# Optimization experiments

Hardware: AMD Instinct MI355X
Metric: run time of the kernel (lower is better)

Reference implementation:

```python
import jax, jax.numpy as jnp
import numpy as np

NUM_EXPERTS = 16
EFF_THRESHOLD = 0.1
SIM_THRESHOLD = 0.0
EPS = 1e-8


def setup_inputs() -> dict:
    key = jax.random.key(0)
    k1, k2 = jax.random.split(key)
    B, E, H = 4096, NUM_EXPERTS, 1024
    rp = jax.random.uniform(k1, (B, E), dtype=jnp.float32)
    rp = rp / rp.sum(axis=-1, keepdims=True)  # valid probabilities
    emb = jax.random.normal(k2, (B, H), dtype=jnp.float32)
    return {"routing_probs": rp, "input_embeddings": emb}


def _total_loss(routing_probs, input_embeddings):
    B, E = routing_probs.shape

    # --- LoadBalanceLoss: var(mean usage) / (1/E)^2, unbiased var (torch default)
    usage = routing_probs.mean(axis=0)                      # [E]
    var = jnp.sum((usage - usage.mean()) ** 2) / (E - 1)
    load_balance = var * (E ** 2)

    # --- EntropyRegularizationLoss (target None): -mean entropy
    entropy = -jnp.sum(routing_probs * jnp.log(routing_probs + EPS), axis=-1)
    entropy_loss = -entropy.mean()

    # --- EfficiencyLoss: sum of probs below threshold, averaged over batch
    small = jnp.where(routing_probs < EFF_THRESHOLD, routing_probs, 0.0)
    efficiency = small.sum(axis=-1).mean()

    # --- ConsistencyLoss: mean KL(softmax(p_j) || softmax(p_i)) over similar pairs
    logp = jax.nn.log_softmax(routing_probs, axis=-1)       # [B, E]
    q = jnp.exp(logp)                                       # [B, E]
    neg_ent_q = jnp.sum(q * logp, axis=-1)                  # [B], = sum q log q
    # KL[i, j] = sum_e q_j (log q_j - logp_i) = neg_ent_q[j] - logp_i . q_j
    kl = neg_ent_q[None, :] - jnp.einsum('ie,je->ij', logp, q)  # [B, B]

    nemb = input_embeddings / jnp.linalg.norm(input_embeddings, axis=-1, keepdims=True)
    sim = nemb @ nemb.T                                     # [B, B]
    mask = (sim > SIM_THRESHOLD) & (~jnp.eye(B, dtype=bool))
    num_pairs = mask.sum()
    cons_sum = jnp.sum(jnp.where(mask, kl, 0.0))
    consistency = jnp.where(num_pairs > 0,
                            cons_sum / jnp.maximum(num_pairs, 1).astype(kl.dtype),
                            0.0)

    return load_balance + entropy_loss + efficiency + consistency


def reference(routing_probs, input_embeddings):
    return _total_loss(routing_probs, input_embeddings)
```

## Files before the change

kernel.cpp:

```cpp
#include <hip/hip_runtime.h>
#include <hip/hip_bf16.h>

#define BROWS 4096
#define NE    16
#define HDIM  1024
#define ACC_F 128
#define NTILE 32
#define NBLK  (NTILE * (NTILE + 1) / 2)

typedef __attribute__((ext_vector_type(8))) short short8;
typedef __attribute__((ext_vector_type(4))) float float4v;

__device__ __forceinline__ unsigned bf16rne(float f) {
    const unsigned u = __float_as_uint(f);
    return (u + 0x7FFFu + ((u >> 16) & 1u)) >> 16;
}
__device__ __forceinline__ unsigned pk2(float lo, float hi) {
    return bf16rne(lo) | (bf16rne(hi) << 16);
}

__device__ __forceinline__ void row16f(const float* src, float* p) {
    const float4v* pv = (const float4v*)src;
    float4v a0 = pv[0], a1 = pv[1], a2 = pv[2], a3 = pv[3];
    p[0]=a0.x; p[1]=a0.y; p[2]=a0.z; p[3]=a0.w;
    p[4]=a1.x; p[5]=a1.y; p[6]=a1.z; p[7]=a1.w;
    p[8]=a2.x; p[9]=a2.y; p[10]=a2.z; p[11]=a2.w;
    p[12]=a3.x; p[13]=a3.y; p[14]=a3.z; p[15]=a3.w;
}

__device__ __forceinline__ void lsm16(const float* p, float* lp, float* q, float& ne) {
    float m = p[0];
#pragma unroll
    for (int e = 1; e < 16; e++) m = fmaxf(m, p[e]);
    float s = 0.f;
#pragma unroll
    for (int e = 0; e < 16; e++) s += expf(p[e] - m);
    const float ls = logf(s);
    ne = 0.f;
#pragma unroll
    for (int e = 0; e < 16; e++) {
        lp[e] = p[e] - m - ls;
        q[e]  = expf(lp[e]);
        ne   += q[e] * lp[e];
    }
}

__device__ __forceinline__ void ldsrow16(const float* base, float* r) {
    float4v a0 = *(const float4v*)(base);
    float4v a1 = *(const float4v*)(base + 4);
    float4v a2 = *(const float4v*)(base + 8);
    float4v a3 = *(const float4v*)(base + 12);
    r[0]=a0.x; r[1]=a0.y; r[2]=a0.z; r[3]=a0.w;
    r[4]=a1.x; r[5]=a1.y; r[6]=a1.z; r[7]=a1.w;
    r[8]=a2.x; r[9]=a2.y; r[10]=a2.z; r[11]=a2.w;
    r[12]=a3.x; r[13]=a3.y; r[14]=a3.z; r[15]=a3.w;
}

__global__ __launch_bounds__(256) void conv_init(
    const float* __restrict__ src, unsigned short* __restrict__ dst, float* __restrict__ acc)
{
    if (blockIdx.x == 0 && threadIdx.x < ACC_F) acc[threadIdx.x] = 0.f;
    const size_t i = ((size_t)blockIdx.x * 256 + threadIdx.x) * 8;
    float4v a = *(const float4v*)(src + i);
    float4v b = *(const float4v*)(src + i + 4);
    uint4 w = {pk2(a.x,a.y), pk2(a.z,a.w), pk2(b.x,b.y), pk2(b.z,b.w)};
    *(uint4*)(dst + i) = w;
}

__device__ __forceinline__ void decode_pair(int id, int& bi, int& bj) {
    int L = (id & 7) * 66 + (id >> 3);
    int gi = 0, gj = 0;
    for (;;) {
        const int cnt = (gi == gj) ? 10 : 16;
        if (L < cnt) break;
        L -= cnt;
        gj++; if (gj == 8) { gi++; gj = gi; }
    }
    if (gi == gj) {
        int u = 0, c = 4;
        while (L >= c) { L -= c; u++; c--; }
        bi = gi * 4 + u; bj = gj * 4 + u + L;
    } else {
        bi = gi * 4 + (L >> 2); bj = gj * 4 + (L & 3);
    }
}

template<bool PRE>
__global__ __launch_bounds__(512, 4) void gram_kl(
    const float* __restrict__ embf, const unsigned short* __restrict__ embb,
    const float* __restrict__ rp, float* __restrict__ acc,
    unsigned int* __restrict__ out)
{
    __shared__ char smem[40960];
    __shared__ float red[16];
    __shared__ int islast;
    __shared__ float fin[96];
    __hip_bfloat16* tA = (__hip_bfloat16*)smem;
    __hip_bfloat16* tB = (__hip_bfloat16*)(smem + 8192);
    float* lpI = (float*)smem;
    float* qI  = (float*)(smem + 10240);
    float* lpJ = (float*)(smem + 20480);
    float* qJ  = (float*)(smem + 30720);

    int bi, bj;
    decode_pair((int)blockIdx.x, bi, bj);

    const int t = threadIdx.x;
    const int lane = t & 63, wid = t >> 6;
    const int wi0 = (wid >> 1) * 32, wj0 = (wid & 1) * 64;
    const int lrow = lane & 15, quad = lane >> 4;

    const int row = t >> 2, cp = t & 3;
    const int sw  = cp ^ ((row >> 1) & 3);
    const int off = row * 32 + sw * 8;

    float4v accf[2][4];
#pragma unroll
    for (int a = 0; a < 2; a++)
#pragma unroll
        for (int b = 0; b < 4; b++) { accf[a][b].x=0.f; accf[a][b].y=0.f; accf[a][b].z=0.f; accf[a][b].w=0.f; }

    int roA[2], roB[4];
#pragma unroll
    for (int f = 0; f < 2; f++) {
        const int ra = wi0 + f * 16 + lrow;
        roA[f] = ra * 32 + (quad ^ ((ra >> 1) & 3)) * 8;
    }
#pragma unroll
    for (int f = 0; f < 4; f++) {
        const int rb = wj0 + f * 16 + lrow;
        roB[f] = rb * 32 + (quad ^ ((rb >> 1) & 3)) * 8;
    }

    if (PRE) {
        const unsigned short* gA = embb + (size_t)(bi * 128) * HDIM;
        const unsigned short* gB = embb + (size_t)(bj * 128) * HDIM;
        uint4 va = *(const uint4*)(gA + (size_t)row * HDIM + cp * 8);
        uint4 vb = *(const uint4*)(gB + (size_t)row * HDIM + cp * 8);
        for (int kt = 0; kt < HDIM; kt += 32) {
            __syncthreads();
            *(uint4*)(tA + off) = va;
            *(uint4*)(tB + off) = vb;
            __syncthreads();
            const int kn = (kt + 32 < HDIM) ? (kt + 32) : kt;
            va = *(const uint4*)(gA + (size_t)row * HDIM + kn + cp * 8);
            vb = *(const uint4*)(gB + (size_t)row * HDIM + kn + cp * 8);
            short8 a[2], b[4];
#pragma unroll
            for (int f = 0; f < 2; f++) a[f] = *(const short8*)(tA + roA[f]);
#pragma unroll
            for (int f = 0; f < 4; f++) b[f] = *(const short8*)(tB + roB[f]);
#pragma unroll
            for (int fi = 0; fi < 2; fi++)
#pragma unroll
                for (int fj = 0; fj < 4; fj++)
                    accf[fi][fj] = __builtin_amdgcn_mfma_f32_16x16x32_bf16(
                        a[fi], b[fj], accf[fi][fj], 0, 0, 0);
        }
    } else {
        const float* gA = embf + (size_t)(bi * 128) * HDIM;
        const float* gB = embf + (size_t)(bj * 128) * HDIM;
        float4v a0, a1, b0, b1;
        {
            const float* pa = gA + (size_t)row * HDIM + cp * 8;
            const float* pb = gB + (size_t)row * HDIM + cp * 8;
            a0 = *(const float4v*)pa; a1 = *(const float4v*)(pa + 4);
            b0 = *(const float4v*)pb; b1 = *(const float4v*)(pb + 4);
        }
        for (int kt = 0; kt < HDIM; kt += 32) {
            uint4 wa = {pk2(a0.x,a0.y), pk2(a0.z,a0.w), pk2(a1.x,a1.y), pk2(a1.z,a1.w)};
            uint4 wb = {pk2(b0.x,b0.y), pk2(b0.z,b0.w), pk2(b1.x,b1.y), pk2(b1.z,b1.w)};
            __syncthreads();
            *(uint4*)(tA + off) = wa;
            *(uint4*)(tB + off) = wb;
            __syncthreads();
            const int kn = (kt + 32 < HDIM) ? (kt + 32) : kt;
            const float* pa = gA + (size_t)row * HDIM + kn + cp * 8;
            const float* pb = gB + (size_t)row * HDIM + kn + cp * 8;
            a0 = *(const float4v*)pa; a1 = *(const float4v*)(pa + 4);
            b0 = *(const float4v*)pb; b1 = *(const float4v*)(pb + 4);
            short8 a[2], b[4];
#pragma unroll
            for (int f = 0; f < 2; f++) a[f] = *(const short8*)(tA + roA[f]);
#pragma unroll
            for (int f = 0; f < 4; f++) b[f] = *(const short8*)(tB + roB[f]);
#pragma unroll
            for (int fi = 0; fi < 2; fi++)
#pragma unroll
                for (int fj = 0; fj < 4; fj++)
                    accf[fi][fj] = __builtin_amdgcn_mfma_f32_16x16x32_bf16(
                        a[fi], b[fj], accf[fi][fj], 0, 0, 0);
        }
    }
    __syncthreads();

    {
        float p[16], lp[16], q[16], ne;
        const bool iSide = (t < 128);
        if (t < 256) {
            const int rloc = iSide ? t : (t - 128);
            const int grow = (iSide ? bi : bj) * 128 + rloc;
            row16f(rp + (size_t)grow * NE, p);
            lsm16(p, lp, q, ne);
            float* dl = (iSide ? lpI : lpJ) + rloc * 20;
            float* dq = (iSide ? qI  : qJ ) + rloc * 20;
            float4v l0 = {lp[0],lp[1],lp[2],lp[3]},   l1 = {lp[4],lp[5],lp[6],lp[7]};
            float4v l2 = {lp[8],lp[9],lp[10],lp[11]}, l3 = {lp[12],lp[13],lp[14],lp[15]};
            *(float4v*)dl = l0; *(float4v*)(dl+4) = l1; *(float4v*)(dl+8) = l2; *(float4v*)(dl+12) = l3;
            float4v q0 = {q[0],q[1],q[2],q[3]},   q1 = {q[4],q[5],q[6],q[7]};
            float4v q2 = {q[8],q[9],q[10],q[11]}, q3 = {q[12],q[13],q[14],q[15]};
            *(float4v*)dq = q0; *(float4v*)(dq+4) = q1; *(float4v*)(dq+8) = q2; *(float4v*)(dq+12) = q3;
            dq[16] = ne;
        }
        if (bi == bj && iSide) {
            float ent = 0.f, eff = 0.f;
#pragma unroll
            for (int e = 0; e < 16; e++) {
                ent += p[e] * logf(p[e] + 1e-8f);
                if (p[e] < 0.1f) eff += p[e];
            }
#pragma unroll
            for (int e = 0; e < 18; e++) {
                float v = (e < 16) ? p[e] : ((e == 16) ? ent : eff);
#pragma unroll
                for (int off2 = 32; off2 > 0; off2 >>= 1) v += __shfl_down(v, off2);
                if (lane == 0) atomicAdd(&acc[e], v);
            }
        }
    }
    __syncthreads();

    float klacc = 0.f, cntacc = 0.f;

    {
        float qreg[4][16], nereg[4];
        int jg[4];
#pragma unroll
        for (int fj = 0; fj < 4; fj++) {
            const int jc = wj0 + fj * 16 + lrow;
            ldsrow16(qJ + jc * 20, qreg[fj]);
            nereg[fj] = qJ[jc * 20 + 16];
            jg[fj] = bj * 128 + jc;
        }
#pragma unroll
        for (int fi = 0; fi < 2; fi++) {
#pragma unroll
            for (int rg = 0; rg < 4; rg++) {
                const int rr = wi0 + fi * 16 + quad * 4 + rg;
                float lpr[16];
                ldsrow16(lpI + rr * 20, lpr);
                const int ig = bi * 128 + rr;
#pragma unroll
                for (int fj = 0; fj < 4; fj++) {
                    float d = 0.f;
#pragma unroll
                    for (int e = 0; e < 16; e++) d += lpr[e] * qreg[fj][e];
                    const float g = accf[fi][fj][rg];
                    if ((g > 0.f) && (ig != jg[fj])) { klacc += nereg[fj] - d; cntacc += 1.f; }
                }
            }
        }
    }

    if (bi != bj) {
        float lpjr[4][16];
#pragma unroll
        for (int fj = 0; fj < 4; fj++) {
            const int jc = wj0 + fj * 16 + lrow;
            ldsrow16(lpJ + jc * 20, lpjr[fj]);
        }
#pragma unroll
        for (int fi = 0; fi < 2; fi++) {
#pragma unroll
            for (int rg = 0; rg < 4; rg++) {
                const int rr = wi0 + fi * 16 + quad * 4 + rg;
                float qrow[16];
                ldsrow16(qI + rr * 20, qrow);
                const float nei = qI[rr * 20 + 16];
#pragma unroll
                for (int fj = 0; fj < 4; fj++) {
                    float d = 0.f;
#pragma unroll
                    for (int e = 0; e < 16; e++) d += lpjr[fj][e] * qrow[e];
                    const float g = accf[fi][fj][rg];
                    if (g > 0.f) { klacc += nei - d; cntacc += 1.f; }
                }
            }
        }
    }

#pragma unroll
    for (int off2 = 32; off2 > 0; off2 >>= 1) {
        klacc  += __shfl_down(klacc, off2);
        cntacc += __shfl_down(cntacc, off2);
    }
    if (lane == 0) { red[wid] = klacc; red[8 + wid] = cntacc; }
    __syncthreads();
    if (t == 0) {
        float k = 0.f, c = 0.f;
#pragma unroll
        for (int w = 0; w < 8; w++) { k += red[w]; c += red[8 + w]; }
        atomicAdd(&acc[18 + ((int)blockIdx.x & 31)], k);
        atomicAdd(&acc[50 + ((int)blockIdx.x & 31)], c);
        const unsigned got = __hip_atomic_fetch_add((unsigned int*)(acc + 82), 1u,
                                                    __ATOMIC_RELEASE, __HIP_MEMORY_SCOPE_AGENT);
        islast = (got == NBLK - 1) ? 1 : 0;
    }
    __syncthreads();

    if (islast) {
        if (t == 0)
            (void)__hip_atomic_load((unsigned int*)(acc + 82), __ATOMIC_ACQUIRE,
                                    __HIP_MEMORY_SCOPE_AGENT);
        __syncthreads();
        if (t < 82)
            fin[t] = __hip_atomic_load(&acc[t], __ATOMIC_RELAXED, __HIP_MEMORY_SCOPE_AGENT);
        __syncthreads();
        if (t == 0) {
            float u[16], usum = 0.f;
#pragma unroll
            for (int e = 0; e < 16; e++) { u[e] = fin[e] / (float)BROWS; usum += u[e]; }
            const float mean = usum / 16.f;
            float var = 0.f;
#pragma unroll
            for (int e = 0; e < 16; e++) { float dd = u[e] - mean; var += dd * dd; }
            var /= 15.f;
            const float lb  = var * 256.f;
            const float ent = fin[16] / (float)BROWS;
            const float eff = fin[17] / (float)BROWS;
            float kl = 0.f, cnt = 0.f;
#pragma unroll
            for (int s = 0; s < 32; s++) { kl += fin[18 + s]; cnt += fin[50 + s]; }
            const float cons = (cnt > 0.f) ? (kl / fmaxf(cnt, 1.f)) : 0.f;
            const float total = lb + ent + eff + cons;
            const unsigned fb   = __float_as_uint(total);
            const unsigned hi   = fb >> 16;
            const unsigned mant = fb & 0xFFFFu;
            const unsigned rnd  = (mant > 0x8000u || (mant == 0x8000u && (hi & 1))) ? 1u : 0u;
            out[0] = (fb & 0xFFFF0000u) | ((hi + rnd) & 0xFFFFu);
        }
    }
}

extern "C" void kernel_launch(void* const* d_in, const int* in_sizes, int n_in,
                              void* d_out, int out_size, void* d_ws, size_t ws_size,
                              hipStream_t stream) {
    const float* rp  = (const float*)d_in[0];
    const float* emb = (const float*)d_in[1];
    float* acc = (float*)d_ws;
    unsigned short* embb = (unsigned short*)((char*)d_ws + ACC_F * sizeof(float));
    (void)in_sizes; (void)n_in; (void)out_size;

    const size_t need = ACC_F * sizeof(float) + (size_t)BROWS * HDIM * 2;
    const bool pre = (ws_size >= need);

    if (pre) {
        conv_init<<<(BROWS * HDIM) / (256 * 8), 256, 0, stream>>>(emb, embb, acc);
        gram_kl<true><<<NBLK, 512, 0, stream>>>(emb, embb, rp, acc, (unsigned int*)d_out);
    } else {
        conv_init<<<1, 256, 0, stream>>>(emb, embb, acc);
        gram_kl<false><<<NBLK, 512, 0, stream>>>(emb, (const unsigned short*)nullptr, rp, acc,
                                                 (unsigned int*)d_out);
    }
}
```

Measured before the change: 125.7 us.

## Compute pairwise KL terms with bf16 MFMA and unroll the K loop by two

The per-pair KL dot products were computed with scalar FP32 FMAs from LDS rows. They are now folded into augmented bf16 vectors (logp with a constant 1, and -q with neg-entropy), so one MFMA per tile yields the KL for each direction. The bf16 prefetch loop is also unrolled to two 32-wide K stages per iteration with double register prefetch. This trades KL precision for bf16 rounding of logp/q, which could change the loss slightly, and the LDS footprint shrinks.

```diff
diff --git a/kernel.cpp b/kernel.cpp
--- a/kernel.cpp
+++ b/kernel.cpp
@@ -43,17 +43,6 @@
         q[e]  = expf(lp[e]);
         ne   += q[e] * lp[e];
     }
-}
-
-__device__ __forceinline__ void ldsrow16(const float* base, float* r) {
-    float4v a0 = *(const float4v*)(base);
-    float4v a1 = *(const float4v*)(base + 4);
-    float4v a2 = *(const float4v*)(base + 8);
-    float4v a3 = *(const float4v*)(base + 12);
-    r[0]=a0.x; r[1]=a0.y; r[2]=a0.z; r[3]=a0.w;
-    r[4]=a1.x; r[5]=a1.y; r[6]=a1.z; r[7]=a1.w;
-    r[8]=a2.x; r[9]=a2.y; r[10]=a2.z; r[11]=a2.w;
-    r[12]=a3.x; r[13]=a3.y; r[14]=a3.z; r[15]=a3.w;
 }
 
 __global__ __launch_bounds__(256) void conv_init(
@@ -91,16 +80,16 @@
     const float* __restrict__ rp, float* __restrict__ acc,
     unsigned int* __restrict__ out)
 {
-    __shared__ char smem[40960];
+    __shared__ char smem[32768];
     __shared__ float red[16];
     __shared__ int islast;
     __shared__ float fin[96];
     __hip_bfloat16* tA = (__hip_bfloat16*)smem;
     __hip_bfloat16* tB = (__hip_bfloat16*)(smem + 8192);
-    float* lpI = (float*)smem;
-    float* qI  = (float*)(smem + 10240);
-    float* lpJ = (float*)(smem + 20480);
-    float* qJ  = (float*)(smem + 30720);
+    __hip_bfloat16* eAF = (__hip_bfloat16*)smem;
+    __hip_bfloat16* eBF = (__hip_bfloat16*)(smem + 8192);
+    __hip_bfloat16* eAR = (__hip_bfloat16*)(smem + 16384);
+    __hip_bfloat16* eBR = (__hip_bfloat16*)(smem + 24576);
 
     int bi, bj;
     decode_pair((int)blockIdx.x, bi, bj);
@@ -133,29 +122,57 @@
     }
 
     if (PRE) {
-        const unsigned short* gA = embb + (size_t)(bi * 128) * HDIM;
-        const unsigned short* gB = embb + (size_t)(bj * 128) * HDIM;
-        uint4 va = *(const uint4*)(gA + (size_t)row * HDIM + cp * 8);
-        uint4 vb = *(const uint4*)(gB + (size_t)row * HDIM + cp * 8);
-        for (int kt = 0; kt < HDIM; kt += 32) {
-            __syncthreads();
-            *(uint4*)(tA + off) = va;
-            *(uint4*)(tB + off) = vb;
-            __syncthreads();
-            const int kn = (kt + 32 < HDIM) ? (kt + 32) : kt;
-            va = *(const uint4*)(gA + (size_t)row * HDIM + kn + cp * 8);
-            vb = *(const uint4*)(gB + (size_t)row * HDIM + kn + cp * 8);
-            short8 a[2], b[4];
-#pragma unroll
-            for (int f = 0; f < 2; f++) a[f] = *(const short8*)(tA + roA[f]);
-#pragma unroll
-            for (int f = 0; f < 4; f++) b[f] = *(const short8*)(tB + roB[f]);
-#pragma unroll
-            for (int fi = 0; fi < 2; fi++)
-#pragma unroll
-                for (int fj = 0; fj < 4; fj++)
-                    accf[fi][fj] = __builtin_amdgcn_mfma_f32_16x16x32_bf16(
-                        a[fi], b[fj], accf[fi][fj], 0, 0, 0);
+        const unsigned short* gA = embb + (size_t)(bi * 128) * HDIM + (size_t)row * HDIM + cp * 8;
+        const unsigned short* gB = embb + (size_t)(bj * 128) * HDIM + (size_t)row * HDIM + cp * 8;
+        uint4 va0 = *(const uint4*)(gA);
+        uint4 vb0 = *(const uint4*)(gB);
+        uint4 va1 = *(const uint4*)(gA + 32);
+        uint4 vb1 = *(const uint4*)(gB + 32);
+        for (int kt = 0; kt < HDIM; kt += 64) {
+            __syncthreads();
+            *(uint4*)(tA + off) = va0;
+            *(uint4*)(tB + off) = vb0;
+            __syncthreads();
+            {
+                const int kn = (kt + 64 < HDIM) ? (kt + 64) : kt;
+                va0 = *(const uint4*)(gA + kn);
+                vb0 = *(const uint4*)(gB + kn);
+            }
+            {
+                short8 a[2], b[4];
+#pragma unroll
+                for (int f = 0; f < 2; f++) a[f] = *(const short8*)(tA + roA[f]);
+#pragma unroll
+                for (int f = 0; f < 4; f++) b[f] = *(const short8*)(tB + roB[f]);
+#pragma unroll
+                for (int fi = 0; fi < 2; fi++)
+#pragma unroll
+                    for (int fj = 0; fj < 4; fj++)
+                        accf[fi][fj] = __builtin_amdgcn_mfma_f32_16x16x32_bf16(
+                            a[fi], b[fj], accf[fi][fj], 0, 0, 0);
+            }
+            __syncthreads();
+            *(uint4*)(tA + off) = va1;
+            *(uint4*)(tB + off) = vb1;
+            __syncthreads();
+            {
+                const int kn = (kt + 96 < HDIM) ? (kt + 96) : (kt + 32);
+                va1 = *(const uint4*)(gA + kn);
+                vb1 = *(const uint4*)(gB + kn);
+            }
+            {
+                short8 a[2], b[4];
+#pragma unroll
+                for (int f = 0; f < 2; f++) a[f] = *(const short8*)(tA + roA[f]);
+#pragma unroll
+                for (int f = 0; f < 4; f++) b[f] = *(const short8*)(tB + roB[f]);
+#pragma unroll
+                for (int fi = 0; fi < 2; fi++)
+#pragma unroll
+                    for (int fj = 0; fj < 4; fj++)
+                        accf[fi][fj] = __builtin_amdgcn_mfma_f32_16x16x32_bf16(
+                            a[fi], b[fj], accf[fi][fj], 0, 0, 0);
+            }
         }
     } else {
         const float* gA = embf + (size_t)(bi * 128) * HDIM;
@@ -202,15 +219,34 @@
             const int grow = (iSide ? bi : bj) * 128 + rloc;
             row16f(rp + (size_t)grow * NE, p);
             lsm16(p, lp, q, ne);
-            float* dl = (iSide ? lpI : lpJ) + rloc * 20;
-            float* dq = (iSide ? qI  : qJ ) + rloc * 20;
-            float4v l0 = {lp[0],lp[1],lp[2],lp[3]},   l1 = {lp[4],lp[5],lp[6],lp[7]};
-            float4v l2 = {lp[8],lp[9],lp[10],lp[11]}, l3 = {lp[12],lp[13],lp[14],lp[15]};
-            *(float4v*)dl = l0; *(float4v*)(dl+4) = l1; *(float4v*)(dl+8) = l2; *(float4v*)(dl+12) = l3;
-            float4v q0 = {q[0],q[1],q[2],q[3]},   q1 = {q[4],q[5],q[6],q[7]};
-            float4v q2 = {q[8],q[9],q[10],q[11]}, q3 = {q[12],q[13],q[14],q[15]};
-            *(float4v*)dq = q0; *(float4v*)(dq+4) = q1; *(float4v*)(dq+8) = q2; *(float4v*)(dq+12) = q3;
-            dq[16] = ne;
+            float r1[16], r2[16], x1, x2;
+            if (iSide) {
+#pragma unroll
+                for (int e = 0; e < 16; e++) { r1[e] = lp[e]; r2[e] = q[e]; }
+                x1 = 1.f; x2 = ne;
+            } else {
+#pragma unroll
+                for (int e = 0; e < 16; e++) { r1[e] = -q[e]; r2[e] = -lp[e]; }
+                x1 = ne; x2 = 1.f;
+            }
+            const int s = (rloc >> 1) & 3;
+            __hip_bfloat16* d1 = (iSide ? eAF : eBF) + rloc * 32;
+            __hip_bfloat16* d2 = (iSide ? eAR : eBR) + rloc * 32;
+            uint4 w0 = {pk2(r1[0],r1[1]), pk2(r1[2],r1[3]), pk2(r1[4],r1[5]), pk2(r1[6],r1[7])};
+            uint4 w1 = {pk2(r1[8],r1[9]), pk2(r1[10],r1[11]), pk2(r1[12],r1[13]), pk2(r1[14],r1[15])};
+            uint4 w2 = {pk2(x1, 0.f), 0u, 0u, 0u};
+            uint4 w3 = {0u, 0u, 0u, 0u};
+            *(uint4*)(d1 + (0 ^ s) * 8) = w0;
+            *(uint4*)(d1 + (1 ^ s) * 8) = w1;
+            *(uint4*)(d1 + (2 ^ s) * 8) = w2;
+            *(uint4*)(d1 + (3 ^ s) * 8) = w3;
+            uint4 v0 = {pk2(r2[0],r2[1]), pk2(r2[2],r2[3]), pk2(r2[4],r2[5]), pk2(r2[6],r2[7])};
+            uint4 v1 = {pk2(r2[8],r2[9]), pk2(r2[10],r2[11]), pk2(r2[12],r2[13]), pk2(r2[14],r2[15])};
+            uint4 v2 = {pk2(x2, 0.f), 0u, 0u, 0u};
+            *(uint4*)(d2 + (0 ^ s) * 8) = v0;
+            *(uint4*)(d2 + (1 ^ s) * 8) = v1;
+            *(uint4*)(d2 + (2 ^ s) * 8) = v2;
+            *(uint4*)(d2 + (3 ^ s) * 8) = w3;
         }
         if (bi == bj && iSide) {
             float ent = 0.f, eff = 0.f;
@@ -230,60 +266,44 @@
     }
     __syncthreads();
 
+    float4v accF[2][4], accR[2][4];
+    {
+        const float4v z = {0.f, 0.f, 0.f, 0.f};
+        short8 af[2], ar[2], bfr[4], brr[4];
+#pragma unroll
+        for (int f = 0; f < 2; f++) {
+            af[f] = *(const short8*)(eAF + roA[f]);
+            ar[f] = *(const short8*)(eAR + roA[f]);
+        }
+#pragma unroll
+        for (int f = 0; f < 4; f++) {
+            bfr[f] = *(const short8*)(eBF + roB[f]);
+            brr[f] = *(const short8*)(eBR + roB[f]);
+        }
+#pragma unroll
+        for (int fi = 0; fi < 2; fi++)
+#pragma unroll
+            for (int fj = 0; fj < 4; fj++) {
+                accF[fi][fj] = __builtin_amdgcn_mfma_f32_16x16x32_bf16(af[fi], bfr[fj], z, 0, 0, 0);
+                accR[fi][fj] = __builtin_amdgcn_mfma_f32_16x16x32_bf16(ar[fi], brr[fj], z, 0, 0, 0);
+            }
+    }
+
     float klacc = 0.f, cntacc = 0.f;
-
-    {
-        float qreg[4][16], nereg[4];
-        int jg[4];
+    const bool offd = (bi != bj);
+#pragma unroll
+    for (int fi = 0; fi < 2; fi++) {
 #pragma unroll
         for (int fj = 0; fj < 4; fj++) {
-            const int jc = wj0 + fj * 16 + lrow;
-            ldsrow16(qJ + jc * 20, qreg[fj]);
-            nereg[fj] = qJ[jc * 20 + 16];
-            jg[fj] = bj * 128 + jc;
-        }
-#pragma unroll
-        for (int fi = 0; fi < 2; fi++) {
 #pragma unroll
             for (int rg = 0; rg < 4; rg++) {
-                const int rr = wi0 + fi * 16 + quad * 4 + rg;
-                float lpr[16];
-                ldsrow16(lpI + rr * 20, lpr);
-                const int ig = bi * 128 + rr;
-#pragma unroll
-                for (int fj = 0; fj < 4; fj++) {
-                    float d = 0.f;
-#pragma unroll
-                    for (int e = 0; e < 16; e++) d += lpr[e] * qreg[fj][e];
-                    const float g = accf[fi][fj][rg];
-                    if ((g > 0.f) && (ig != jg[fj])) { klacc += nereg[fj] - d; cntacc += 1.f; }
-                }
-            }
-        }
-    }
-
-    if (bi != bj) {
-        float lpjr[4][16];
-#pragma unroll
-        for (int fj = 0; fj < 4; fj++) {
-            const int jc = wj0 + fj * 16 + lrow;
-            ldsrow16(lpJ + jc * 20, lpjr[fj]);
-        }
-#pragma unroll
-        for (int fi = 0; fi < 2; fi++) {
-#pragma unroll
-            for (int rg = 0; rg < 4; rg++) {
-                const int rr = wi0 + fi * 16 + quad * 4 + rg;
-                float qrow[16];
-                ldsrow16(qI + rr * 20, qrow);
-                const float nei = qI[rr * 20 + 16];
-#pragma unroll
-                for (int fj = 0; fj < 4; fj++) {
-                    float d = 0.f;
-#pragma unroll
-                    for (int e = 0; e < 16; e++) d += lpjr[fj][e] * qrow[e];
-                    const float g = accf[fi][fj][rg];
-                    if (g > 0.f) { klacc += nei - d; cntacc += 1.f; }
+                const int ig = bi * 128 + wi0 + fi * 16 + quad * 4 + rg;
+                const int jg = bj * 128 + wj0 + fj * 16 + lrow;
+                const float g = accf[fi][fj][rg];
+                if ((g > 0.f) && (ig != jg)) {
+                    klacc  += accF[fi][fj][rg];
+                    cntacc += 1.f;
+                    if (offd) { klacc += accR[fi][fj][rg]; cntacc += 1.f; }
                 }
             }
         }
```

Measured after the change: 117.9 us. 1.07x faster.

## Run per-wave 64x64 tiles from global loads and compute KL via MFMA

Applied to the files above, without the earlier changes.

Each block now holds four independent waves, each computing a 64x64 Gram sub-tile by loading bf16 fragments straight from global memory into registers with double buffering. This drops the shared-memory staging and block barriers. The KL cross term is rebuilt as an augmented bf16 matrix product (log-probs with a ones column times negated q with the neg-entropy column) on MFMA, replacing the scalar 16-wide dot loops. The similarity mask is packed into a 64-bit mask, and completion is tracked per wave with a ticket counter. Risks: bf16 rounding of the KL operands reduces precision, global fragment loads are less coalesced, and diagonal blocks leave one wave idle.

```diff
diff --git a/kernel.cpp b/kernel.cpp
--- a/kernel.cpp
+++ b/kernel.cpp
@@ -5,8 +5,9 @@
 #define NE    16
 #define HDIM  1024
 #define ACC_F 128
-#define NTILE 32
-#define NBLK  (NTILE * (NTILE + 1) / 2)
+#define NSUP  32
+#define NBLK  (NSUP * (NSUP + 1) / 2)
+#define NTICK (NBLK * 4)
 
 typedef __attribute__((ext_vector_type(8))) short short8;
 typedef __attribute__((ext_vector_type(4))) float float4v;
@@ -45,15 +46,17 @@
     }
 }
 
-__device__ __forceinline__ void ldsrow16(const float* base, float* r) {
-    float4v a0 = *(const float4v*)(base);
-    float4v a1 = *(const float4v*)(base + 4);
-    float4v a2 = *(const float4v*)(base + 8);
-    float4v a3 = *(const float4v*)(base + 12);
-    r[0]=a0.x; r[1]=a0.y; r[2]=a0.z; r[3]=a0.w;
-    r[4]=a1.x; r[5]=a1.y; r[6]=a1.z; r[7]=a1.w;
-    r[8]=a2.x; r[9]=a2.y; r[10]=a2.z; r[11]=a2.w;
-    r[12]=a3.x; r[13]=a3.y; r[14]=a3.z; r[15]=a3.w;
+__device__ __forceinline__ void wrow(__hip_bfloat16* tile, int row, const float* v, float x) {
+    __hip_bfloat16* d = tile + row * 32;
+    const int s = (row >> 1) & 3;
+    uint4 w0 = {pk2(v[0],v[1]),  pk2(v[2],v[3]),   pk2(v[4],v[5]),   pk2(v[6],v[7])};
+    uint4 w1 = {pk2(v[8],v[9]),  pk2(v[10],v[11]), pk2(v[12],v[13]), pk2(v[14],v[15])};
+    uint4 w2 = {pk2(x, 0.f), 0u, 0u, 0u};
+    uint4 w3 = {0u, 0u, 0u, 0u};
+    *(uint4*)(d + (0 ^ s) * 8) = w0;
+    *(uint4*)(d + (1 ^ s) * 8) = w1;
+    *(uint4*)(d + (2 ^ s) * 8) = w2;
+    *(uint4*)(d + (3 ^ s) * 8) = w3;
 }
 
 __global__ __launch_bounds__(256) void conv_init(
@@ -86,252 +89,227 @@
 }
 
 template<bool PRE>
-__global__ __launch_bounds__(512, 4) void gram_kl(
+__global__ __launch_bounds__(256, 3) void gram_kl(
     const float* __restrict__ embf, const unsigned short* __restrict__ embb,
     const float* __restrict__ rp, float* __restrict__ acc,
     unsigned int* __restrict__ out)
 {
-    __shared__ char smem[40960];
-    __shared__ float red[16];
-    __shared__ int islast;
-    __shared__ float fin[96];
-    __hip_bfloat16* tA = (__hip_bfloat16*)smem;
-    __hip_bfloat16* tB = (__hip_bfloat16*)(smem + 8192);
-    float* lpI = (float*)smem;
-    float* qI  = (float*)(smem + 10240);
-    float* lpJ = (float*)(smem + 20480);
-    float* qJ  = (float*)(smem + 30720);
-
-    int bi, bj;
-    decode_pair((int)blockIdx.x, bi, bj);
-
-    const int t = threadIdx.x;
-    const int lane = t & 63, wid = t >> 6;
-    const int wi0 = (wid >> 1) * 32, wj0 = (wid & 1) * 64;
+    __shared__ __hip_bfloat16 aug[4][2][2048];
+
+    int BI, BJ;
+    decode_pair((int)blockIdx.x, BI, BJ);
+
+    const int t = threadIdx.x, lane = t & 63, wid = t >> 6;
     const int lrow = lane & 15, quad = lane >> 4;
-
-    const int row = t >> 2, cp = t & 3;
-    const int sw  = cp ^ ((row >> 1) & 3);
-    const int off = row * 32 + sw * 8;
-
-    float4v accf[2][4];
-#pragma unroll
-    for (int a = 0; a < 2; a++)
-#pragma unroll
-        for (int b = 0; b < 4; b++) { accf[a][b].x=0.f; accf[a][b].y=0.f; accf[a][b].z=0.f; accf[a][b].w=0.f; }
-
-    int roA[2], roB[4];
-#pragma unroll
-    for (int f = 0; f < 2; f++) {
-        const int ra = wi0 + f * 16 + lrow;
-        roA[f] = ra * 32 + (quad ^ ((ra >> 1) & 3)) * 8;
-    }
-#pragma unroll
-    for (int f = 0; f < 4; f++) {
-        const int rb = wj0 + f * 16 + lrow;
-        roB[f] = rb * 32 + (quad ^ ((rb >> 1) & 3)) * 8;
-    }
-
-    if (PRE) {
-        const unsigned short* gA = embb + (size_t)(bi * 128) * HDIM;
-        const unsigned short* gB = embb + (size_t)(bj * 128) * HDIM;
-        uint4 va = *(const uint4*)(gA + (size_t)row * HDIM + cp * 8);
-        uint4 vb = *(const uint4*)(gB + (size_t)row * HDIM + cp * 8);
-        for (int kt = 0; kt < HDIM; kt += 32) {
-            __syncthreads();
-            *(uint4*)(tA + off) = va;
-            *(uint4*)(tB + off) = vb;
-            __syncthreads();
-            const int kn = (kt + 32 < HDIM) ? (kt + 32) : kt;
-            va = *(const uint4*)(gA + (size_t)row * HDIM + kn + cp * 8);
-            vb = *(const uint4*)(gB + (size_t)row * HDIM + kn + cp * 8);
-            short8 a[2], b[4];
-#pragma unroll
-            for (int f = 0; f < 2; f++) a[f] = *(const short8*)(tA + roA[f]);
-#pragma unroll
-            for (int f = 0; f < 4; f++) b[f] = *(const short8*)(tB + roB[f]);
-#pragma unroll
-            for (int fi = 0; fi < 2; fi++)
-#pragma unroll
-                for (int fj = 0; fj < 4; fj++)
-                    accf[fi][fj] = __builtin_amdgcn_mfma_f32_16x16x32_bf16(
-                        a[fi], b[fj], accf[fi][fj], 0, 0, 0);
-        }
-    } else {
-        const float* gA = embf + (size_t)(bi * 128) * HDIM;
-        const float* gB = embf + (size_t)(bj * 128) * HDIM;
-        float4v a0, a1, b0, b1;
+    const int bi = BI * 2 + (wid >> 1), bj = BJ * 2 + (wid & 1);
+    const bool idle = (BI == BJ) && (wid == 2);
+    const bool dg = (bi == bj);
+
+    float klacc = 0.f, cntacc = 0.f;
+
+    if (!idle) {
+        float4v accg[4][4];
+#pragma unroll
+        for (int a = 0; a < 4; a++)
+#pragma unroll
+            for (int b = 0; b < 4; b++) { accg[a][b].x=0.f; accg[a][b].y=0.f; accg[a][b].z=0.f; accg[a][b].w=0.f; }
+
+        if (PRE) {
+            const unsigned short* pa[4];
+            const unsigned short* pb[4];
+#pragma unroll
+            for (int f = 0; f < 4; f++) {
+                pa[f] = embb + (size_t)(bi * 64 + f * 16 + lrow) * HDIM + quad * 8;
+                pb[f] = embb + (size_t)(bj * 64 + f * 16 + lrow) * HDIM + quad * 8;
+            }
+            short8 a0[4], b0[4], a1[4], b1[4];
+#pragma unroll
+            for (int f = 0; f < 4; f++) { a0[f] = *(const short8*)(pa[f]);      b0[f] = *(const short8*)(pb[f]); }
+#pragma unroll
+            for (int f = 0; f < 4; f++) { a1[f] = *(const short8*)(pa[f] + 32); b1[f] = *(const short8*)(pb[f] + 32); }
+            for (int kt = 0; kt < HDIM; kt += 64) {
+#pragma unroll
+                for (int fi = 0; fi < 4; fi++)
+#pragma unroll
+                    for (int fj = 0; fj < 4; fj++)
+                        accg[fi][fj] = __builtin_amdgcn_mfma_f32_16x16x32_bf16(
+                            a0[fi], b0[fj], accg[fi][fj], 0, 0, 0);
+                const int kn0 = (kt + 64 < HDIM) ? (kt + 64) : kt;
+#pragma unroll
+                for (int f = 0; f < 4; f++) { a0[f] = *(const short8*)(pa[f] + kn0); b0[f] = *(const short8*)(pb[f] + kn0); }
+#pragma unroll
+                for (int fi = 0; fi < 4; fi++)
+#pragma unroll
+                    for (int fj = 0; fj < 4; fj++)
+                        accg[fi][fj] = __builtin_amdgcn_mfma_f32_16x16x32_bf16(
+                            a1[fi], b1[fj], accg[fi][fj], 0, 0, 0);
+                const int kn1 = (kt + 96 < HDIM) ? (kt + 96) : (kt + 32);
+#pragma unroll
+                for (int f = 0; f < 4; f++) { a1[f] = *(const short8*)(pa[f] + kn1); b1[f] = *(const short8*)(pb[f] + kn1); }
+            }
+        } else {
+            const float* pa[4];
+            const float* pb[4];
+#pragma unroll
+            for (int f = 0; f < 4; f++) {
+                pa[f] = embf + (size_t)(bi * 64 + f * 16 + lrow) * HDIM + quad * 8;
+                pb[f] = embf + (size_t)(bj * 64 + f * 16 + lrow) * HDIM + quad * 8;
+            }
+            for (int kt = 0; kt < HDIM; kt += 32) {
+                short8 a[4], b[4];
+#pragma unroll
+                for (int f = 0; f < 4; f++) {
+                    float4v x = *(const float4v*)(pa[f] + kt), y = *(const float4v*)(pa[f] + kt + 4);
+                    uint4 w = {pk2(x.x,x.y), pk2(x.z,x.w), pk2(y.x,y.y), pk2(y.z,y.w)};
+                    a[f] = *(short8*)&w;
+                    float4v u = *(const float4v*)(pb[f] + kt), v = *(const float4v*)(pb[f] + kt + 4);
+                    uint4 w2 = {pk2(u.x,u.y), pk2(u.z,u.w), pk2(v.x,v.y), pk2(v.z,v.w)};
+                    b[f] = *(short8*)&w2;
+                }
+#pragma unroll
+                for (int fi = 0; fi < 4; fi++)
+#pragma unroll
+                    for (int fj = 0; fj < 4; fj++)
+                        accg[fi][fj] = __builtin_amdgcn_mfma_f32_16x16x32_bf16(
+                            a[fi], b[fj], accg[fi][fj], 0, 0, 0);
+            }
+        }
+
+        unsigned long long msk = 0ull;
+#pragma unroll
+        for (int fi = 0; fi < 4; fi++)
+#pragma unroll
+            for (int fj = 0; fj < 4; fj++)
+#pragma unroll
+                for (int rg = 0; rg < 4; rg++) {
+                    const bool self = dg && (fi == fj) && ((quad * 4 + rg) == lrow);
+                    if ((accg[fi][fj][rg] > 0.f) && !self)
+                        msk |= (1ull << ((fi * 4 + fj) * 4 + rg));
+                }
+        cntacc = (float)__popcll(msk) * (dg ? 1.f : 2.f);
+
+        __hip_bfloat16* eA = &aug[wid][0][0];
+        __hip_bfloat16* eB = &aug[wid][1][0];
+        int lro[4];
+#pragma unroll
+        for (int f = 0; f < 4; f++) {
+            const int r = f * 16 + lrow;
+            lro[f] = r * 32 + (quad ^ ((r >> 1) & 3)) * 8;
+        }
+
+        float qI[16], lpJ[16], neI;
         {
-            const float* pa = gA + (size_t)row * HDIM + cp * 8;
-            const float* pb = gB + (size_t)row * HDIM + cp * 8;
-            a0 = *(const float4v*)pa; a1 = *(const float4v*)(pa + 4);
-            b0 = *(const float4v*)pb; b1 = *(const float4v*)(pb + 4);
-        }
-        for (int kt = 0; kt < HDIM; kt += 32) {
-            uint4 wa = {pk2(a0.x,a0.y), pk2(a0.z,a0.w), pk2(a1.x,a1.y), pk2(a1.z,a1.w)};
-            uint4 wb = {pk2(b0.x,b0.y), pk2(b0.z,b0.w), pk2(b1.x,b1.y), pk2(b1.z,b1.w)};
-            __syncthreads();
-            *(uint4*)(tA + off) = wa;
-            *(uint4*)(tB + off) = wb;
-            __syncthreads();
-            const int kn = (kt + 32 < HDIM) ? (kt + 32) : kt;
-            const float* pa = gA + (size_t)row * HDIM + kn + cp * 8;
-            const float* pb = gB + (size_t)row * HDIM + kn + cp * 8;
-            a0 = *(const float4v*)pa; a1 = *(const float4v*)(pa + 4);
-            b0 = *(const float4v*)pb; b1 = *(const float4v*)(pb + 4);
-            short8 a[2], b[4];
-#pragma unroll
-            for (int f = 0; f < 2; f++) a[f] = *(const short8*)(tA + roA[f]);
-#pragma unroll
-            for (int f = 0; f < 4; f++) b[f] = *(const short8*)(tB + roB[f]);
-#pragma unroll
-            for (int fi = 0; fi < 2; fi++)
-#pragma unroll
-                for (int fj = 0; fj < 4; fj++)
-                    accf[fi][fj] = __builtin_amdgcn_mfma_f32_16x16x32_bf16(
-                        a[fi], b[fj], accf[fi][fj], 0, 0, 0);
-        }
-    }
-    __syncthreads();
-
-    {
-        float p[16], lp[16], q[16], ne;
-        const bool iSide = (t < 128);
-        if (t < 256) {
-            const int rloc = iSide ? t : (t - 128);
-            const int grow = (iSide ? bi : bj) * 128 + rloc;
-            row16f(rp + (size_t)grow * NE, p);
-            lsm16(p, lp, q, ne);
-            float* dl = (iSide ? lpI : lpJ) + rloc * 20;
-            float* dq = (iSide ? qI  : qJ ) + rloc * 20;
-            float4v l0 = {lp[0],lp[1],lp[2],lp[3]},   l1 = {lp[4],lp[5],lp[6],lp[7]};
-            float4v l2 = {lp[8],lp[9],lp[10],lp[11]}, l3 = {lp[12],lp[13],lp[14],lp[15]};
-            *(float4v*)dl = l0; *(float4v*)(dl+4) = l1; *(float4v*)(dl+8) = l2; *(float4v*)(dl+12) = l3;
-            float4v q0 = {q[0],q[1],q[2],q[3]},   q1 = {q[4],q[5],q[6],q[7]};
-            float4v q2 = {q[8],q[9],q[10],q[11]}, q3 = {q[12],q[13],q[14],q[15]};
-            *(float4v*)dq = q0; *(float4v*)(dq+4) = q1; *(float4v*)(dq+8) = q2; *(float4v*)(dq+12) = q3;
-            dq[16] = ne;
-        }
-        if (bi == bj && iSide) {
-            float ent = 0.f, eff = 0.f;
-#pragma unroll
-            for (int e = 0; e < 16; e++) {
-                ent += p[e] * logf(p[e] + 1e-8f);
-                if (p[e] < 0.1f) eff += p[e];
-            }
-#pragma unroll
-            for (int e = 0; e < 18; e++) {
-                float v = (e < 16) ? p[e] : ((e == 16) ? ent : eff);
-#pragma unroll
-                for (int off2 = 32; off2 > 0; off2 >>= 1) v += __shfl_down(v, off2);
-                if (lane == 0) atomicAdd(&acc[e], v);
-            }
-        }
-    }
-    __syncthreads();
-
-    float klacc = 0.f, cntacc = 0.f;
-
-    {
-        float qreg[4][16], nereg[4];
-        int jg[4];
-#pragma unroll
-        for (int fj = 0; fj < 4; fj++) {
-            const int jc = wj0 + fj * 16 + lrow;
-            ldsrow16(qJ + jc * 20, qreg[fj]);
-            nereg[fj] = qJ[jc * 20 + 16];
-            jg[fj] = bj * 128 + jc;
-        }
-#pragma unroll
-        for (int fi = 0; fi < 2; fi++) {
-#pragma unroll
-            for (int rg = 0; rg < 4; rg++) {
-                const int rr = wi0 + fi * 16 + quad * 4 + rg;
-                float lpr[16];
-                ldsrow16(lpI + rr * 20, lpr);
-                const int ig = bi * 128 + rr;
+            float p[16], lp[16], ne;
+            row16f(rp + (size_t)(bi * 64 + lane) * NE, p);
+            lsm16(p, lp, qI, neI);
+            if (dg) {
+                float ent = 0.f, eff = 0.f;
+#pragma unroll
+                for (int e = 0; e < 16; e++) {
+                    ent += p[e] * logf(p[e] + 1e-8f);
+                    if (p[e] < 0.1f) eff += p[e];
+                }
+#pragma unroll
+                for (int e = 0; e < 18; e++) {
+                    float v = (e < 16) ? p[e] : ((e == 16) ? ent : eff);
+#pragma unroll
+                    for (int o = 32; o > 0; o >>= 1) v += __shfl_down(v, o);
+                    if (lane == 0) atomicAdd(&acc[e], v);
+                }
+            }
+            wrow(eA, lane, lp, 1.f);
+            float pj[16], qj[16], nej;
+            row16f(rp + (size_t)(bj * 64 + lane) * NE, pj);
+            lsm16(pj, lpJ, qj, nej);
+            float nq[16];
+#pragma unroll
+            for (int e = 0; e < 16; e++) nq[e] = -qj[e];
+            wrow(eB, lane, nq, nej);
+        }
+        __threadfence_block();
+        {
+            const float4v z = {0.f, 0.f, 0.f, 0.f};
+            short8 af[4], bf[4];
+#pragma unroll
+            for (int f = 0; f < 4; f++) { af[f] = *(const short8*)(eA + lro[f]); bf[f] = *(const short8*)(eB + lro[f]); }
+#pragma unroll
+            for (int fi = 0; fi < 4; fi++)
 #pragma unroll
                 for (int fj = 0; fj < 4; fj++) {
-                    float d = 0.f;
-#pragma unroll
-                    for (int e = 0; e < 16; e++) d += lpr[e] * qreg[fj][e];
-                    const float g = accf[fi][fj][rg];
-                    if ((g > 0.f) && (ig != jg[fj])) { klacc += nereg[fj] - d; cntacc += 1.f; }
-                }
-            }
-        }
-    }
-
-    if (bi != bj) {
-        float lpjr[4][16];
-#pragma unroll
-        for (int fj = 0; fj < 4; fj++) {
-            const int jc = wj0 + fj * 16 + lrow;
-            ldsrow16(lpJ + jc * 20, lpjr[fj]);
-        }
-#pragma unroll
-        for (int fi = 0; fi < 2; fi++) {
-#pragma unroll
-            for (int rg = 0; rg < 4; rg++) {
-                const int rr = wi0 + fi * 16 + quad * 4 + rg;
-                float qrow[16];
-                ldsrow16(qI + rr * 20, qrow);
-                const float nei = qI[rr * 20 + 16];
+                    float4v r = __builtin_amdgcn_mfma_f32_16x16x32_bf16(af[fi], bf[fj], z, 0, 0, 0);
+#pragma unroll
+                    for (int rg = 0; rg < 4; rg++)
+                        if ((msk >> ((fi * 4 + fj) * 4 + rg)) & 1ull) klacc += r[rg];
+                }
+        }
+
+        if (!dg) {
+            __threadfence_block();
+            wrow(eA, lane, qI, neI);
+            float nl[16];
+#pragma unroll
+            for (int e = 0; e < 16; e++) nl[e] = -lpJ[e];
+            wrow(eB, lane, nl, 1.f);
+            __threadfence_block();
+            const float4v z = {0.f, 0.f, 0.f, 0.f};
+            short8 af[4], bf[4];
+#pragma unroll
+            for (int f = 0; f < 4; f++) { af[f] = *(const short8*)(eA + lro[f]); bf[f] = *(const short8*)(eB + lro[f]); }
+#pragma unroll
+            for (int fi = 0; fi < 4; fi++)
 #pragma unroll
                 for (int fj = 0; fj < 4; fj++) {
-                    float d = 0.f;
-#pragma unroll
-                    for (int e = 0; e < 16; e++) d += lpjr[fj][e] * qrow[e];
-                    const float g = accf[fi][fj][rg];
-                    if (g > 0.f) { klacc += nei - d; cntacc += 1.f; }
-                }
-            }
-        }
-    }
-
-#pragma unroll
-    for (int off2 = 32; off2 > 0; off2 >>= 1) {
-        klacc  += __shfl_down(klacc, off2);
-        cntacc += __shfl_down(cntacc, off2);
-    }
-    if (lane == 0) { red[wid] = klacc; red[8 + wid] = cntacc; }
-    __syncthreads();
-    if (t == 0) {
-        float k = 0.f, c = 0.f;
-#pragma unroll
-        for (int w = 0; w < 8; w++) { k += red[w]; c += red[8 + w]; }
-        atomicAdd(&acc[18 + ((int)blockIdx.x & 31)], k);
-        atomicAdd(&acc[50 + ((int)blockIdx.x & 31)], c);
-        const unsigned got = __hip_atomic_fetch_add((unsigned int*)(acc + 82), 1u,
-                                                    __ATOMIC_RELEASE, __HIP_MEMORY_SCOPE_AGENT);
-        islast = (got == NBLK - 1) ? 1 : 0;
-    }
-    __syncthreads();
-
-    if (islast) {
-        if (t == 0)
-            (void)__hip_atomic_load((unsigned int*)(acc + 82), __ATOMIC_ACQUIRE,
-                                    __HIP_MEMORY_SCOPE_AGENT);
-        __syncthreads();
-        if (t < 82)
-            fin[t] = __hip_atomic_load(&acc[t], __ATOMIC_RELAXED, __HIP_MEMORY_SCOPE_AGENT);
-        __syncthreads();
-        if (t == 0) {
-            float u[16], usum = 0.f;
-#pragma unroll
-            for (int e = 0; e < 16; e++) { u[e] = fin[e] / (float)BROWS; usum += u[e]; }
-            const float mean = usum / 16.f;
-            float var = 0.f;
-#pragma unroll
-            for (int e = 0; e < 16; e++) { float dd = u[e] - mean; var += dd * dd; }
-            var /= 15.f;
-            const float lb  = var * 256.f;
-            const float ent = fin[16] / (float)BROWS;
-            const float eff = fin[17] / (float)BROWS;
-            float kl = 0.f, cnt = 0.f;
-#pragma unroll
-            for (int s = 0; s < 32; s++) { kl += fin[18 + s]; cnt += fin[50 + s]; }
-            const float cons = (cnt > 0.f) ? (kl / fmaxf(cnt, 1.f)) : 0.f;
+                    float4v r = __builtin_amdgcn_mfma_f32_16x16x32_bf16(af[fi], bf[fj], z, 0, 0, 0);
+#pragma unroll
+                    for (int rg = 0; rg < 4; rg++)
+                        if ((msk >> ((fi * 4 + fj) * 4 + rg)) & 1ull) klacc += r[rg];
+                }
+        }
+
+#pragma unroll
+        for (int o = 32; o > 0; o >>= 1) {
+            klacc  += __shfl_down(klacc, o);
+            cntacc += __shfl_down(cntacc, o);
+        }
+        if (lane == 0) {
+            const int slot = ((int)blockIdx.x * 4 + wid) & 31;
+            atomicAdd(&acc[18 + slot], klacc);
+            atomicAdd(&acc[50 + slot], cntacc);
+        }
+    }
+
+    unsigned got = 0u;
+    if (lane == 0)
+        got = __hip_atomic_fetch_add((unsigned int*)(acc + 82), 1u,
+                                     __ATOMIC_RELEASE, __HIP_MEMORY_SCOPE_AGENT);
+    got = __shfl(got, 0);
+
+    if (got == NTICK - 1) {
+        (void)__hip_atomic_load((unsigned int*)(acc + 82), __ATOMIC_ACQUIRE,
+                                __HIP_MEMORY_SCOPE_AGENT);
+        const float v0 = __hip_atomic_load(&acc[lane],      __ATOMIC_RELAXED, __HIP_MEMORY_SCOPE_AGENT);
+        const float v1 = __hip_atomic_load(&acc[lane + 64], __ATOMIC_RELAXED, __HIP_MEMORY_SCOPE_AGENT);
+        float us = (lane < 16) ? v0 : 0.f;
+#pragma unroll
+        for (int o = 32; o > 0; o >>= 1) us += __shfl_xor(us, o);
+        const float mean = us / (float)BROWS / 16.f;
+        float dv = (lane < 16) ? (v0 / (float)BROWS - mean) : 0.f;
+        dv = dv * dv;
+        float var = (lane < 16) ? dv : 0.f;
+#pragma unroll
+        for (int o = 32; o > 0; o >>= 1) var += __shfl_xor(var, o);
+        var /= 15.f;
+        float kls = (lane >= 18 && lane < 50) ? v0 : 0.f;
+#pragma unroll
+        for (int o = 32; o > 0; o >>= 1) kls += __shfl_xor(kls, o);
+        float cns = ((lane >= 50) ? v0 : 0.f) + ((lane < 18) ? v1 : 0.f);
+#pragma unroll
+        for (int o = 32; o > 0; o >>= 1) cns += __shfl_xor(cns, o);
+        const float ent = __shfl(v0, 16) / (float)BROWS;
+        const float eff = __shfl(v0, 17) / (float)BROWS;
+        if (lane == 0) {
+            const float lb   = var * 256.f;
+            const float cons = (cns > 0.f) ? (kls / fmaxf(cns, 1.f)) : 0.f;
             const float total = lb + ent + eff + cons;
             const unsigned fb   = __float_as_uint(total);
             const unsigned hi   = fb >> 16;
@@ -356,10 +334,10 @@
 
     if (pre) {
         conv_init<<<(BROWS * HDIM) / (256 * 8), 256, 0, stream>>>(emb, embb, acc);
-        gram_kl<true><<<NBLK, 512, 0, stream>>>(emb, embb, rp, acc, (unsigned int*)d_out);
+        gram_kl<true><<<NBLK, 256, 0, stream>>>(emb, embb, rp, acc, (unsigned int*)d_out);
     } else {
         conv_init<<<1, 256, 0, stream>>>(emb, embb, acc);
-        gram_kl<false><<<NBLK, 512, 0, stream>>>(emb, (const unsigned short*)nullptr, rp, acc,
+        gram_kl<false><<<NBLK, 256, 0, stream>>>(emb, (const unsigned short*)nullptr, rp, acc,
                                                  (unsigned int*)d_out);
     }
 }
```

Measured after the change: 185.3 us. 1.47x slower.
